# Kernel optimization log

Measured on AMD Instinct MI355X. Metric: run time of the kernel, lower is better.

The kernel has to match this reference:

```python
import jax, jax.numpy as jnp
import numpy as np

P = 16          # patch size
ER = 2          # expand_ratio = per-head dim in Hgru2

def _shift2d(x, sh, sw):
    # zero-fill shift of (B,C,H,W) image by (sh, sw); matches torch F.pad((l,r,t,b)) with a negative crop
    H, W = x.shape[2], x.shape[3]
    ah, aw = abs(sh), abs(sw)
    xp = jnp.pad(x, ((0, 0), (0, 0), (ah, ah), (aw, aw)))
    return xp[:, :, ah - sh:ah - sh + H, aw - sw:aw - sw + W]

def _layernorm(x, g, b, eps=1e-5):
    m = jnp.mean(x, axis=-1, keepdims=True)
    v = jnp.var(x, axis=-1, keepdims=True)
    return (x - m) * jax.lax.rsqrt(v + eps) * g + b

def _rmsnorm(x, eps=1e-6):
    # FastSimpleRMSNorm: weightless RMS normalization
    return x * jax.lax.rsqrt(jnp.mean(x * x, axis=-1, keepdims=True) + eps)

def _hgru2(x, lb_vec, wi, wo):
    # x: (N, T, D). NOTE: the torch module unpacks x.shape as (n, b, d), so the
    # gated linear recurrence scans over axis 0 exactly as the original does.
    N, T, D = x.shape
    H = D // ER
    feat = x @ wi                                    # (N, T, 3D)
    V, Q, Fg = jnp.split(feat, 3, axis=-1)
    V = jax.nn.gelu(V, approximate=False).reshape(N, T, H, ER)
    Q = jax.nn.gelu(Q, approximate=False).reshape(N, T, H, ER)
    Fg = jax.nn.sigmoid(Fg).reshape(N, T, H, ER)
    lb = lb_vec.reshape(H, ER)
    lam = lb + (1.0 - lb) * Fg                       # decay lambda_t in (lb, 1)
    K = 1.0 - lam
    def step(S, inp):
        q, k, v, l = inp                             # each (T, H, ER)
        # S[t,h,i,j] = lam[i] * S + k[i] * v[j]  (GLA recurrence, 2x2 state/head)
        S = l[..., None] * S + k[..., None] * v[..., None, :]
        o = jnp.einsum('thi,thij->thj', q, S)
        return S, o
    S0 = jnp.zeros((T, H, ER, ER), dtype=x.dtype)
    _, o = jax.lax.scan(step, S0, (Q, K, V, lam))    # o: (N, T, H, ER)
    return o.reshape(N, T, D) @ wo

def reference(img, spt_ln_g, spt_ln_b, spt_w, spt_b, pos_emb, cls_token, lower_bounds,
              in_proj_w, out_proj_w, ff_w1, ff_b1, ff_w2, ff_b2,
              head_ln_g, head_ln_b, head_w, head_b):
    B, C, Hh, Ww = img.shape
    # SPT: concat original + 4 shifted copies on channel axis -> (B, 5C, H, W)
    xs = jnp.concatenate([img,
                          _shift2d(img, 0, 1), _shift2d(img, 0, -1),
                          _shift2d(img, 1, 0), _shift2d(img, -1, 0)], axis=1)
    c5 = 5 * C
    h, w = Hh // P, Ww // P
    # 'b c (h p1) (w p2) -> b (h w) (p1 p2 c)'
    patches = xs.reshape(B, c5, h, P, w, P).transpose(0, 2, 4, 3, 5, 1).reshape(B, h * w, P * P * c5)
    tokens = _layernorm(patches, spt_ln_g, spt_ln_b) @ spt_w + spt_b   # (B, NP, D)
    n = tokens.shape[1]
    cls = jnp.broadcast_to(cls_token, (B, 1, tokens.shape[2]))
    x = jnp.concatenate([cls, tokens], axis=1) + pos_emb[:, :n + 1]
    # layer-wise monotone lower bounds for the decay gate
    lb = jax.nn.softmax(lower_bounds, axis=0)
    lb = jnp.cumsum(lb, axis=0)
    lb = lb - lb[0]
    depth = lower_bounds.shape[0]
    for i in range(depth):
        x = _hgru2(_rmsnorm(x), lb[i], in_proj_w[i], out_proj_w[i]) + x
        hmid = jax.nn.gelu(_rmsnorm(x) @ ff_w1[i] + ff_b1[i], approximate=False)
        x = hmid @ ff_w2[i] + ff_b2[i] + x
    x = _rmsnorm(x)
    x = x[:, 0]                                      # cls pooling
    return _layernorm(x, head_ln_g, head_ln_b) @ head_w + head_b

def setup_inputs():
    key = jax.random.key(0)
    ks = jax.random.split(key, 10)
    B, C, IMG, D, DEPTH, MLP, NC = 16, 3, 256, 768, 8, 3072, 1000
    NP = (IMG // P) ** 2
    PD = P * P * 5 * C
    s = 0.02
    return {
        'img': jax.random.normal(ks[0], (B, C, IMG, IMG), jnp.float32),
        'spt_ln_g': jnp.ones((PD,), jnp.float32),
        'spt_ln_b': jnp.zeros((PD,), jnp.float32),
        'spt_w': jax.random.normal(ks[1], (PD, D), jnp.float32) * s,
        'spt_b': jnp.zeros((D,), jnp.float32),
        'pos_emb': jax.random.normal(ks[2], (1, NP + 1, D), jnp.float32),
        'cls_token': jax.random.normal(ks[3], (1, 1, D), jnp.float32),
        'lower_bounds': jnp.ones((DEPTH, D), jnp.float32),
        'in_proj_w': jax.random.normal(ks[4], (DEPTH, D, 3 * D), jnp.float32) * s,
        'out_proj_w': jax.random.normal(ks[5], (DEPTH, D, D), jnp.float32) * s,
        'ff_w1': jax.random.normal(ks[6], (DEPTH, D, MLP), jnp.float32) * s,
        'ff_b1': jnp.zeros((DEPTH, MLP), jnp.float32),
        'ff_w2': jax.random.normal(ks[7], (DEPTH, MLP, D), jnp.float32) * s,
        'ff_b2': jnp.zeros((DEPTH, D), jnp.float32),
        'head_ln_g': jnp.ones((D,), jnp.float32),
        'head_ln_b': jnp.zeros((D,), jnp.float32),
        'head_w': jax.random.normal(ks[8], (D, NC), jnp.float32) * s,
        'head_b': jnp.zeros((NC,), jnp.float32),
    }
```

## Files before the change

### kernel.cpp

```cpp
#include <hip/hip_runtime.h>
#include <hip/hip_bf16.h>

typedef __bf16 bf16x8 __attribute__((ext_vector_type(8)));
typedef float floatx4 __attribute__((ext_vector_type(4)));

#define DEV __device__ __forceinline__

DEV float gelu_f(float x) {
    return 0.5f * x * (1.0f + erff(x * 0.70710678118654752f));
}

DEV void block_reduce2(float& a, float& b, float* s) {
    #pragma unroll
    for (int o = 32; o > 0; o >>= 1) {
        a += __shfl_down(a, o, 64);
        b += __shfl_down(b, o, 64);
    }
    __syncthreads();
    int wv = threadIdx.x >> 6;
    if ((threadIdx.x & 63) == 0) { s[wv * 2] = a; s[wv * 2 + 1] = b; }
    __syncthreads();
    int nw = blockDim.x >> 6;
    float ra = 0.f, rb = 0.f;
    for (int i = 0; i < nw; ++i) { ra += s[i * 2]; rb += s[i * 2 + 1]; }
    a = ra; b = rb;
}

__global__ __launch_bounds__(256) void compute_lb(const float* __restrict__ lbin, float* __restrict__ lbout) {
    int d = blockIdx.x * 256 + threadIdx.x;
    if (d >= 768) return;
    float v[8];
    float mx = -1e30f;
    #pragma unroll
    for (int i = 0; i < 8; ++i) { v[i] = lbin[i * 768 + d]; mx = fmaxf(mx, v[i]); }
    float s = 0.f;
    #pragma unroll
    for (int i = 0; i < 8; ++i) { v[i] = expf(v[i] - mx); s += v[i]; }
    float inv = 1.f / s;
    float first = v[0] * inv;
    float cum = 0.f;
    #pragma unroll
    for (int i = 0; i < 8; ++i) { cum += v[i] * inv; lbout[i * 768 + d] = cum - first; }
}

__global__ __launch_bounds__(256) void init_tokens(const float* __restrict__ cls, const float* __restrict__ pos,
                                                   const float* __restrict__ bias, float* __restrict__ x) {
    int i = blockIdx.x * 256 + threadIdx.x;
    if (i >= 16 * 257 * 768) return;
    int d = i % 768;
    int row = i / 768;
    int t = row % 257;
    float v;
    if (t == 0) v = cls[d] + pos[d];
    else        v = bias[d] + pos[(size_t)t * 768 + d];
    x[(size_t)row * 768 + d] = v;
}

__global__ __launch_bounds__(256) void patch_ln(const float* __restrict__ img, const float* __restrict__ g,
                                                const float* __restrict__ bt, __hip_bfloat16* __restrict__ out) {
    int pm = blockIdx.x;
    int b = pm >> 8, pp = pm & 255;
    int ph = pp >> 4, pw = pp & 15;
    __shared__ float pv[3840];
    __shared__ float sbuf[8];
    float s = 0.f, ss = 0.f;
    #pragma unroll
    for (int i = 0; i < 15; ++i) {
        int f = threadIdx.x + i * 256;
        int pi = f / 15, cc = f % 15;
        int ip = pi >> 4, jp = pi & 15;
        int g5 = cc / 3, ch = cc % 3;
        int sh = (g5 == 3) - (g5 == 4);
        int sw = (g5 == 1) - (g5 == 2);
        int y = ph * 16 + ip - sh;
        int x = pw * 16 + jp - sw;
        float val = 0.f;
        if ((unsigned)y < 256u && (unsigned)x < 256u)
            val = img[(((size_t)b * 3 + ch) * 256 + y) * 256 + x];
        pv[f] = val; s += val; ss += val * val;
    }
    block_reduce2(s, ss, sbuf);
    float mean = s * (1.f / 3840.f);
    float var  = ss * (1.f / 3840.f) - mean * mean;
    float inv  = rsqrtf(var + 1e-5f);
    #pragma unroll
    for (int i = 0; i < 15; ++i) {
        int f = threadIdx.x + i * 256;
        out[(size_t)pm * 3840 + f] = __float2bfloat16((pv[f] - mean) * inv * g[f] + bt[f]);
    }
}

__global__ __launch_bounds__(256) void transpose_cast(const float* __restrict__ W, __hip_bfloat16* __restrict__ Wt,
                                                      int K, int N) {
    __shared__ float tile[32][33];
    int k0 = blockIdx.x * 32, n0 = blockIdx.y * 32;
    int tx = threadIdx.x & 31, ty = threadIdx.x >> 5;
    #pragma unroll
    for (int i = 0; i < 4; ++i) {
        int k = ty + i * 8;
        tile[k][tx] = W[(size_t)(k0 + k) * N + n0 + tx];
    }
    __syncthreads();
    #pragma unroll
    for (int i = 0; i < 4; ++i) {
        int n = ty + i * 8;
        Wt[(size_t)(n0 + n) * K + k0 + tx] = __float2bfloat16(tile[tx][n]);
    }
}

__global__ __launch_bounds__(256) void rmsnorm_kernel(const float* __restrict__ x, __hip_bfloat16* __restrict__ out) {
    int row = blockIdx.x;
    const float* xr = x + (size_t)row * 768;
    __shared__ float sbuf[8];
    float v[3];
    float ss = 0.f, d0 = 0.f;
    #pragma unroll
    for (int i = 0; i < 3; ++i) { v[i] = xr[threadIdx.x + i * 256]; ss += v[i] * v[i]; }
    block_reduce2(ss, d0, sbuf);
    float scale = rsqrtf(ss * (1.f / 768.f) + 1e-6f);
    #pragma unroll
    for (int i = 0; i < 3; ++i)
        out[(size_t)row * 768 + threadIdx.x + i * 256] = __float2bfloat16(v[i] * scale);
}

__global__ __launch_bounds__(256) void hgru_scan(const float* __restrict__ feat, __hip_bfloat16* __restrict__ o) {
    int idx = blockIdx.x * 256 + threadIdx.x;
    if (idx >= 257 * 384) return;
    int t = idx / 384, h = idx % 384;
    float S00 = 0.f, S01 = 0.f, S10 = 0.f, S11 = 0.f;
    for (int n = 0; n < 16; ++n) {
        size_t base = ((size_t)n * 257 + t) * 2304;
        float v0 = feat[base + h * 2],        v1 = feat[base + h * 2 + 1];
        float q0 = feat[base + 768 + h * 2],  q1 = feat[base + 768 + h * 2 + 1];
        float l0 = feat[base + 1536 + h * 2], l1 = feat[base + 1536 + h * 2 + 1];
        float k0 = 1.f - l0, k1 = 1.f - l1;
        S00 = l0 * S00 + k0 * v0; S01 = l0 * S01 + k0 * v1;
        S10 = l1 * S10 + k1 * v0; S11 = l1 * S11 + k1 * v1;
        float o0 = q0 * S00 + q1 * S10;
        float o1 = q0 * S01 + q1 * S11;
        size_t ob = ((size_t)n * 257 + t) * 768 + h * 2;
        o[ob]     = __float2bfloat16(o0);
        o[ob + 1] = __float2bfloat16(o1);
    }
}

__global__ __launch_bounds__(256) void head_kernel(const float* __restrict__ x, const float* __restrict__ g,
                                                   const float* __restrict__ be, const float* __restrict__ hw,
                                                   const float* __restrict__ hb, float* __restrict__ out) {
    int b = blockIdx.x;
    const float* xr = x + (size_t)b * 257 * 768;
    __shared__ float z[768];
    __shared__ float sbuf[8];
    float v[3];
    float ss = 0.f, d0 = 0.f;
    #pragma unroll
    for (int i = 0; i < 3; ++i) { v[i] = xr[threadIdx.x + i * 256]; ss += v[i] * v[i]; }
    block_reduce2(ss, d0, sbuf);
    float rs = rsqrtf(ss * (1.f / 768.f) + 1e-6f);
    float s = 0.f, s2 = 0.f;
    #pragma unroll
    for (int i = 0; i < 3; ++i) { float y = v[i] * rs; s += y; s2 += y * y; }
    block_reduce2(s, s2, sbuf);
    float mean = s * (1.f / 768.f);
    float var  = s2 * (1.f / 768.f) - mean * mean;
    float inv  = rsqrtf(var + 1e-5f);
    #pragma unroll
    for (int i = 0; i < 3; ++i) {
        int d = threadIdx.x + i * 256;
        z[d] = (v[i] * rs - mean) * inv * g[d] + be[d];
    }
    __syncthreads();
    int j = blockIdx.y * 256 + threadIdx.x;
    if (j < 1000) {
        float acc = hb[j];
        for (int d = 0; d < 768; ++d) acc += z[d] * hw[d * 1000 + j];
        out[b * 1000 + j] = acc;
    }
}

template<int EPI, int SPLITK>
__global__ __launch_bounds__(256) void gemm_bt(
        const __hip_bfloat16* __restrict__ A, const __hip_bfloat16* __restrict__ Bt,
        int N, int Ktot, int Mvalid,
        float* __restrict__ outf, __hip_bfloat16* __restrict__ outb,
        const float* __restrict__ bias, const float* __restrict__ aux) {
    __shared__ alignas(16) __hip_bfloat16 Als[2][128 * 32];
    __shared__ alignas(16) __hip_bfloat16 Bls[2][128 * 32];
    const int tid  = threadIdx.x;
    const int lane = tid & 63;
    const int wv   = tid >> 6;
    const int m0 = blockIdx.y * 128;
    const int n0 = blockIdx.x * 128;
    const int kLen  = Ktot / SPLITK;
    const int kBase = blockIdx.z * kLen;
    const int wm = wv & 1, wn = wv >> 1;
    const int fr = lane & 15;
    const int fq = lane >> 4;
    const int srow = lane >> 2;
    const int scol = (lane & 3) * 8;

    floatx4 acc[4][4];
    #pragma unroll
    for (int mi = 0; mi < 4; ++mi)
        #pragma unroll
        for (int ni = 0; ni < 4; ++ni)
            acc[mi][ni] = (floatx4){0.f, 0.f, 0.f, 0.f};

    const int c  = wv * 2;
    const int r0 = c * 16 + srow;

    auto stage = [&](int kt, int buf) {
        #pragma unroll
        for (int j = 0; j < 2; ++j) {
            int cc = c + j;
            int r  = r0 + j * 16;
            const __hip_bfloat16* ga = A  + (size_t)(m0 + r) * Ktot + kBase + kt + scol;
            __builtin_amdgcn_global_load_lds((const __attribute__((address_space(1))) void*)ga,
                                             (__attribute__((address_space(3))) void*)(&Als[buf][cc * 512]), 16, 0, 0);
            const __hip_bfloat16* gb = Bt + (size_t)(n0 + r) * Ktot + kBase + kt + scol;
            __builtin_amdgcn_global_load_lds((const __attribute__((address_space(1))) void*)gb,
                                             (__attribute__((address_space(3))) void*)(&Bls[buf][cc * 512]), 16, 0, 0);
        }
    };

    const int nk = kLen / 32;
    stage(0, 0);
    __syncthreads();

    for (int i = 0; i < nk; ++i) {
        const int cur = i & 1;
        bf16x8 af[4], bfv[4];
        #pragma unroll
        for (int mi = 0; mi < 4; ++mi)
            af[mi] = *(const bf16x8*)((const void*)&Als[cur][(wm * 64 + mi * 16 + fr) * 32 + fq * 8]);
        #pragma unroll
        for (int ni = 0; ni < 4; ++ni)
            bfv[ni] = *(const bf16x8*)((const void*)&Bls[cur][(wn * 64 + ni * 16 + fr) * 32 + fq * 8]);
        if (i + 1 < nk) stage((i + 1) * 32, cur ^ 1);
        #pragma unroll
        for (int mi = 0; mi < 4; ++mi)
            #pragma unroll
            for (int ni = 0; ni < 4; ++ni)
                acc[mi][ni] = __builtin_amdgcn_mfma_f32_16x16x32_bf16(af[mi], bfv[ni], acc[mi][ni], 0, 0, 0);
        __syncthreads();
    }

    const int cr0 = wm * 64 + fq * 4;
    const int cc0 = wn * 64 + fr;
    #pragma unroll
    for (int mi = 0; mi < 4; ++mi) {
        #pragma unroll
        for (int r = 0; r < 4; ++r) {
            int gm = m0 + cr0 + mi * 16 + r;
            if (gm >= Mvalid) continue;
            #pragma unroll
            for (int ni = 0; ni < 4; ++ni) {
                int gn = n0 + cc0 + ni * 16;
                float v = acc[mi][ni][r];
                if (EPI == 0) {
                    int b = gm >> 8, p = gm & 255;
                    size_t orow = (size_t)b * 257 + 1 + p;
                    atomicAdd(&outf[orow * 768 + gn], v);
                } else if (EPI == 1) {
                    float res;
                    if (gn < 1536) {
                        res = gelu_f(v);
                    } else {
                        float l = aux[gn - 1536];
                        res = l + (1.f - l) / (1.f + expf(-v));
                    }
                    outf[(size_t)gm * N + gn] = res;
                } else if (EPI == 2) {
                    if (SPLITK > 1) atomicAdd(&outf[(size_t)gm * N + gn], v);
                    else            outf[(size_t)gm * N + gn] += v;
                } else if (EPI == 3) {
                    outb[(size_t)gm * N + gn] = __float2bfloat16(gelu_f(v + bias[gn]));
                } else if (EPI == 4) {
                    float add = v + (blockIdx.z == 0 ? bias[gn] : 0.f);
                    if (SPLITK > 1) atomicAdd(&outf[(size_t)gm * N + gn], add);
                    else            outf[(size_t)gm * N + gn] += add;
                }
            }
        }
    }
}

extern "C" void kernel_launch(void* const* d_in, const int* in_sizes, int n_in,
                              void* d_out, int out_size, void* d_ws, size_t ws_size,
                              hipStream_t stream) {
    const float* img        = (const float*)d_in[0];
    const float* spt_ln_g   = (const float*)d_in[1];
    const float* spt_ln_b   = (const float*)d_in[2];
    const float* spt_w      = (const float*)d_in[3];
    const float* spt_b      = (const float*)d_in[4];
    const float* pos_emb    = (const float*)d_in[5];
    const float* cls_token  = (const float*)d_in[6];
    const float* lower_bnds = (const float*)d_in[7];
    const float* in_proj_w  = (const float*)d_in[8];
    const float* out_proj_w = (const float*)d_in[9];
    const float* ff_w1      = (const float*)d_in[10];
    const float* ff_b1      = (const float*)d_in[11];
    const float* ff_w2      = (const float*)d_in[12];
    const float* ff_b2      = (const float*)d_in[13];
    const float* head_ln_g  = (const float*)d_in[14];
    const float* head_ln_b  = (const float*)d_in[15];
    const float* head_w     = (const float*)d_in[16];
    const float* head_b     = (const float*)d_in[17];
    float* out = (float*)d_out;

    char* wp = (char*)d_ws;
    auto alloc = [&](size_t bytes) -> void* {
        void* p = (void*)wp;
        wp += (bytes + 255) & ~(size_t)255;
        return p;
    };
    float*          lbbuf   = (float*)         alloc(8 * 768 * 4);
    __hip_bfloat16* patches = (__hip_bfloat16*)alloc((size_t)4096 * 3840 * 2);
    __hip_bfloat16* spt_wt  = (__hip_bfloat16*)alloc((size_t)768 * 3840 * 2);
    float*          xbuf    = (float*)         alloc((size_t)4112 * 768 * 4);
    __hip_bfloat16* normbuf = (__hip_bfloat16*)alloc((size_t)4224 * 768 * 2);
    float*          featbuf = (float*)         alloc((size_t)4112 * 2304 * 4);
    __hip_bfloat16* obuf    = (__hip_bfloat16*)alloc((size_t)4224 * 768 * 2);
    __hip_bfloat16* midbuf  = (__hip_bfloat16*)alloc((size_t)4224 * 3072 * 2);
    __hip_bfloat16* w_in_t  = (__hip_bfloat16*)alloc((size_t)2304 * 768 * 2);
    __hip_bfloat16* w_out_t = (__hip_bfloat16*)alloc((size_t)768 * 768 * 2);
    __hip_bfloat16* w1_t    = (__hip_bfloat16*)alloc((size_t)3072 * 768 * 2);
    __hip_bfloat16* w2_t    = (__hip_bfloat16*)alloc((size_t)768 * 3072 * 2);
    (void)in_sizes; (void)n_in; (void)out_size; (void)ws_size;

    compute_lb<<<3, 256, 0, stream>>>(lower_bnds, lbbuf);
    init_tokens<<<(16 * 257 * 768 + 255) / 256, 256, 0, stream>>>(cls_token, pos_emb, spt_b, xbuf);
    patch_ln<<<4096, 256, 0, stream>>>(img, spt_ln_g, spt_ln_b, patches);
    transpose_cast<<<dim3(3840 / 32, 768 / 32), 256, 0, stream>>>(spt_w, spt_wt, 3840, 768);
    gemm_bt<0, 4><<<dim3(6, 32, 4), 256, 0, stream>>>(patches, spt_wt, 768, 3840, 4096,
                                                      xbuf, nullptr, nullptr, nullptr);

    for (int i = 0; i < 8; ++i) {
        rmsnorm_kernel<<<4112, 256, 0, stream>>>(xbuf, normbuf);
        transpose_cast<<<dim3(24, 72), 256, 0, stream>>>(in_proj_w + (size_t)i * 768 * 2304, w_in_t, 768, 2304);
        gemm_bt<1, 1><<<dim3(18, 33, 1), 256, 0, stream>>>(normbuf, w_in_t, 2304, 768, 4112,
                                                           featbuf, nullptr, nullptr, lbbuf + i * 768);
        hgru_scan<<<386, 256, 0, stream>>>(featbuf, obuf);
        transpose_cast<<<dim3(24, 24), 256, 0, stream>>>(out_proj_w + (size_t)i * 768 * 768, w_out_t, 768, 768);
        gemm_bt<2, 2><<<dim3(6, 33, 2), 256, 0, stream>>>(obuf, w_out_t, 768, 768, 4112,
                                                          xbuf, nullptr, nullptr, nullptr);
        rmsnorm_kernel<<<4112, 256, 0, stream>>>(xbuf, normbuf);
        transpose_cast<<<dim3(24, 96), 256, 0, stream>>>(ff_w1 + (size_t)i * 768 * 3072, w1_t, 768, 3072);
        gemm_bt<3, 1><<<dim3(24, 33, 1), 256, 0, stream>>>(normbuf, w1_t, 3072, 768, 4112,
                                                           nullptr, midbuf, ff_b1 + i * 3072, nullptr);
        transpose_cast<<<dim3(96, 24), 256, 0, stream>>>(ff_w2 + (size_t)i * 3072 * 768, w2_t, 3072, 768);
        gemm_bt<4, 4><<<dim3(6, 33, 4), 256, 0, stream>>>(midbuf, w2_t, 768, 3072, 4112,
                                                          xbuf, nullptr, ff_b2 + i * 768, nullptr);
    }

    head_kernel<<<dim3(16, 4), 256, 0, stream>>>(xbuf, head_ln_g, head_ln_b, head_w, head_b, out);
}
```

Baseline: 2.200 ms.

## Register-staged swizzled GEMM pipeline, bf16 feature buffer, narrower out-proj tiles

The GEMM now loads the next-but-one k-tile into registers and writes it to XOR-swizzled LDS after the MFMAs, replacing the direct global-to-LDS loads. This is meant to overlap global latency with compute and avoid LDS bank conflicts. The tile width NT becomes a template parameter, so the out-proj GEMM runs with 64-wide N tiles on twice as many blocks. The in-proj epilogue writes bf16 features instead of fp32, and the scan reads them as bf16 pairs, halving that traffic at some cost in precision for the gates and values.

```diff
diff --git a/kernel.cpp b/kernel.cpp
--- a/kernel.cpp
+++ b/kernel.cpp
@@ -123,16 +123,20 @@
         out[(size_t)row * 768 + threadIdx.x + i * 256] = __float2bfloat16(v[i] * scale);
 }
 
-__global__ __launch_bounds__(256) void hgru_scan(const float* __restrict__ feat, __hip_bfloat16* __restrict__ o) {
+__global__ __launch_bounds__(256) void hgru_scan(const __hip_bfloat162* __restrict__ feat,
+                                                 __hip_bfloat16* __restrict__ o) {
     int idx = blockIdx.x * 256 + threadIdx.x;
     if (idx >= 257 * 384) return;
     int t = idx / 384, h = idx % 384;
     float S00 = 0.f, S01 = 0.f, S10 = 0.f, S11 = 0.f;
     for (int n = 0; n < 16; ++n) {
-        size_t base = ((size_t)n * 257 + t) * 2304;
-        float v0 = feat[base + h * 2],        v1 = feat[base + h * 2 + 1];
-        float q0 = feat[base + 768 + h * 2],  q1 = feat[base + 768 + h * 2 + 1];
-        float l0 = feat[base + 1536 + h * 2], l1 = feat[base + 1536 + h * 2 + 1];
+        size_t b2 = ((size_t)n * 257 + t) * 1152;
+        __hip_bfloat162 V = feat[b2 + h];
+        __hip_bfloat162 Q = feat[b2 + 384 + h];
+        __hip_bfloat162 L = feat[b2 + 768 + h];
+        float v0 = __bfloat162float(V.x), v1 = __bfloat162float(V.y);
+        float q0 = __bfloat162float(Q.x), q1 = __bfloat162float(Q.y);
+        float l0 = __bfloat162float(L.x), l1 = __bfloat162float(L.y);
         float k0 = 1.f - l0, k1 = 1.f - l1;
         S00 = l0 * S00 + k0 * v0; S01 = l0 * S01 + k0 * v1;
         S10 = l1 * S10 + k1 * v0; S11 = l1 * S11 + k1 * v1;
@@ -178,75 +182,99 @@
     }
 }
 
-template<int EPI, int SPLITK>
+template<int EPI, int SPLITK, int NT>
 __global__ __launch_bounds__(256) void gemm_bt(
         const __hip_bfloat16* __restrict__ A, const __hip_bfloat16* __restrict__ Bt,
         int N, int Ktot, int Mvalid,
         float* __restrict__ outf, __hip_bfloat16* __restrict__ outb,
         const float* __restrict__ bias, const float* __restrict__ aux) {
+    constexpr int NF = NT / 32;
+    constexpr int BJ = NT / 64;
     __shared__ alignas(16) __hip_bfloat16 Als[2][128 * 32];
-    __shared__ alignas(16) __hip_bfloat16 Bls[2][128 * 32];
+    __shared__ alignas(16) __hip_bfloat16 Bls[2][NT * 32];
     const int tid  = threadIdx.x;
     const int lane = tid & 63;
     const int wv   = tid >> 6;
     const int m0 = blockIdx.y * 128;
-    const int n0 = blockIdx.x * 128;
+    const int n0 = blockIdx.x * NT;
     const int kLen  = Ktot / SPLITK;
     const int kBase = blockIdx.z * kLen;
     const int wm = wv & 1, wn = wv >> 1;
     const int fr = lane & 15;
     const int fq = lane >> 4;
-    const int srow = lane >> 2;
-    const int scol = (lane & 3) * 8;
-
-    floatx4 acc[4][4];
+    const int sr = tid >> 2;
+    const int sc = tid & 3;
+
+    floatx4 acc[4][NF];
     #pragma unroll
     for (int mi = 0; mi < 4; ++mi)
         #pragma unroll
-        for (int ni = 0; ni < 4; ++ni)
+        for (int ni = 0; ni < NF; ++ni)
             acc[mi][ni] = (floatx4){0.f, 0.f, 0.f, 0.f};
 
-    const int c  = wv * 2;
-    const int r0 = c * 16 + srow;
-
-    auto stage = [&](int kt, int buf) {
+    int4 ra[2][2], rb[2][BJ];
+
+    auto gload = [&](int kt, int pipe) {
         #pragma unroll
         for (int j = 0; j < 2; ++j) {
-            int cc = c + j;
-            int r  = r0 + j * 16;
-            const __hip_bfloat16* ga = A  + (size_t)(m0 + r) * Ktot + kBase + kt + scol;
-            __builtin_amdgcn_global_load_lds((const __attribute__((address_space(1))) void*)ga,
-                                             (__attribute__((address_space(3))) void*)(&Als[buf][cc * 512]), 16, 0, 0);
-            const __hip_bfloat16* gb = Bt + (size_t)(n0 + r) * Ktot + kBase + kt + scol;
-            __builtin_amdgcn_global_load_lds((const __attribute__((address_space(1))) void*)gb,
-                                             (__attribute__((address_space(3))) void*)(&Bls[buf][cc * 512]), 16, 0, 0);
+            int r = sr + 64 * j;
+            ra[pipe][j] = *(const int4*)(A + (size_t)(m0 + r) * Ktot + kBase + kt + sc * 8);
+        }
+        #pragma unroll
+        for (int j = 0; j < BJ; ++j) {
+            int r = sr + 64 * j;
+            rb[pipe][j] = *(const int4*)(Bt + (size_t)(n0 + r) * Ktot + kBase + kt + sc * 8);
         }
     };
+    auto swz = [&](int row, int chunk) -> int {
+        return row * 64 + ((chunk ^ ((row >> 1) & 3)) * 16);
+    };
+    auto swrite = [&](int pipe, int buf) {
+        #pragma unroll
+        for (int j = 0; j < 2; ++j) {
+            int r = sr + 64 * j;
+            *(int4*)((char*)&Als[buf][0] + swz(r, sc)) = ra[pipe][j];
+        }
+        #pragma unroll
+        for (int j = 0; j < BJ; ++j) {
+            int r = sr + 64 * j;
+            *(int4*)((char*)&Bls[buf][0] + swz(r, sc)) = rb[pipe][j];
+        }
+    };
 
     const int nk = kLen / 32;
-    stage(0, 0);
+    gload(0, 0);
+    if (nk > 1) gload(32, 1);
+    swrite(0, 0);
     __syncthreads();
 
     for (int i = 0; i < nk; ++i) {
         const int cur = i & 1;
-        bf16x8 af[4], bfv[4];
-        #pragma unroll
-        for (int mi = 0; mi < 4; ++mi)
-            af[mi] = *(const bf16x8*)((const void*)&Als[cur][(wm * 64 + mi * 16 + fr) * 32 + fq * 8]);
-        #pragma unroll
-        for (int ni = 0; ni < 4; ++ni)
-            bfv[ni] = *(const bf16x8*)((const void*)&Bls[cur][(wn * 64 + ni * 16 + fr) * 32 + fq * 8]);
-        if (i + 1 < nk) stage((i + 1) * 32, cur ^ 1);
+        if (i + 2 < nk) gload((i + 2) * 32, cur);
+        bf16x8 af[4], bfv[NF];
+        #pragma unroll
+        for (int mi = 0; mi < 4; ++mi) {
+            int row = wm * 64 + mi * 16 + fr;
+            af[mi] = *(const bf16x8*)((const char*)&Als[cur][0] + swz(row, fq));
+        }
+        #pragma unroll
+        for (int ni = 0; ni < NF; ++ni) {
+            int row = wn * (NT / 2) + ni * 16 + fr;
+            bfv[ni] = *(const bf16x8*)((const char*)&Bls[cur][0] + swz(row, fq));
+        }
         #pragma unroll
         for (int mi = 0; mi < 4; ++mi)
             #pragma unroll
-            for (int ni = 0; ni < 4; ++ni)
+            for (int ni = 0; ni < NF; ++ni)
                 acc[mi][ni] = __builtin_amdgcn_mfma_f32_16x16x32_bf16(af[mi], bfv[ni], acc[mi][ni], 0, 0, 0);
-        __syncthreads();
+        if (i + 1 < nk) {
+            swrite(cur ^ 1, cur ^ 1);
+            __syncthreads();
+        }
     }
 
     const int cr0 = wm * 64 + fq * 4;
-    const int cc0 = wn * 64 + fr;
+    const int cc0 = wn * (NT / 2) + fr;
     #pragma unroll
     for (int mi = 0; mi < 4; ++mi) {
         #pragma unroll
@@ -254,7 +282,7 @@
             int gm = m0 + cr0 + mi * 16 + r;
             if (gm >= Mvalid) continue;
             #pragma unroll
-            for (int ni = 0; ni < 4; ++ni) {
+            for (int ni = 0; ni < NF; ++ni) {
                 int gn = n0 + cc0 + ni * 16;
                 float v = acc[mi][ni][r];
                 if (EPI == 0) {
@@ -269,7 +297,7 @@
                         float l = aux[gn - 1536];
                         res = l + (1.f - l) / (1.f + expf(-v));
                     }
-                    outf[(size_t)gm * N + gn] = res;
+                    outb[(size_t)gm * N + gn] = __float2bfloat16(res);
                 } else if (EPI == 2) {
                     if (SPLITK > 1) atomicAdd(&outf[(size_t)gm * N + gn], v);
                     else            outf[(size_t)gm * N + gn] += v;
@@ -319,7 +347,7 @@
     __hip_bfloat16* spt_wt  = (__hip_bfloat16*)alloc((size_t)768 * 3840 * 2);
     float*          xbuf    = (float*)         alloc((size_t)4112 * 768 * 4);
     __hip_bfloat16* normbuf = (__hip_bfloat16*)alloc((size_t)4224 * 768 * 2);
-    float*          featbuf = (float*)         alloc((size_t)4112 * 2304 * 4);
+    __hip_bfloat16* featbuf = (__hip_bfloat16*)alloc((size_t)4112 * 2304 * 2);
     __hip_bfloat16* obuf    = (__hip_bfloat16*)alloc((size_t)4224 * 768 * 2);
     __hip_bfloat16* midbuf  = (__hip_bfloat16*)alloc((size_t)4224 * 3072 * 2);
     __hip_bfloat16* w_in_t  = (__hip_bfloat16*)alloc((size_t)2304 * 768 * 2);
@@ -332,25 +360,25 @@
     init_tokens<<<(16 * 257 * 768 + 255) / 256, 256, 0, stream>>>(cls_token, pos_emb, spt_b, xbuf);
     patch_ln<<<4096, 256, 0, stream>>>(img, spt_ln_g, spt_ln_b, patches);
     transpose_cast<<<dim3(3840 / 32, 768 / 32), 256, 0, stream>>>(spt_w, spt_wt, 3840, 768);
-    gemm_bt<0, 4><<<dim3(6, 32, 4), 256, 0, stream>>>(patches, spt_wt, 768, 3840, 4096,
-                                                      xbuf, nullptr, nullptr, nullptr);
+    gemm_bt<0, 4, 128><<<dim3(6, 32, 4), 256, 0, stream>>>(patches, spt_wt, 768, 3840, 4096,
+                                                           xbuf, nullptr, nullptr, nullptr);
 
     for (int i = 0; i < 8; ++i) {
         rmsnorm_kernel<<<4112, 256, 0, stream>>>(xbuf, normbuf);
         transpose_cast<<<dim3(24, 72), 256, 0, stream>>>(in_proj_w + (size_t)i * 768 * 2304, w_in_t, 768, 2304);
-        gemm_bt<1, 1><<<dim3(18, 33, 1), 256, 0, stream>>>(normbuf, w_in_t, 2304, 768, 4112,
-                                                           featbuf, nullptr, nullptr, lbbuf + i * 768);
-        hgru_scan<<<386, 256, 0, stream>>>(featbuf, obuf);
+        gemm_bt<1, 1, 128><<<dim3(18, 33, 1), 256, 0, stream>>>(normbuf, w_in_t, 2304, 768, 4112,
+                                                                nullptr, featbuf, nullptr, lbbuf + i * 768);
+        hgru_scan<<<386, 256, 0, stream>>>((const __hip_bfloat162*)featbuf, obuf);
         transpose_cast<<<dim3(24, 24), 256, 0, stream>>>(out_proj_w + (size_t)i * 768 * 768, w_out_t, 768, 768);
-        gemm_bt<2, 2><<<dim3(6, 33, 2), 256, 0, stream>>>(obuf, w_out_t, 768, 768, 4112,
-                                                          xbuf, nullptr, nullptr, nullptr);
+        gemm_bt<2, 2, 64><<<dim3(12, 33, 2), 256, 0, stream>>>(obuf, w_out_t, 768, 768, 4112,
+                                                               xbuf, nullptr, nullptr, nullptr);
         rmsnorm_kernel<<<4112, 256, 0, stream>>>(xbuf, normbuf);
         transpose_cast<<<dim3(24, 96), 256, 0, stream>>>(ff_w1 + (size_t)i * 768 * 3072, w1_t, 768, 3072);
-        gemm_bt<3, 1><<<dim3(24, 33, 1), 256, 0, stream>>>(normbuf, w1_t, 3072, 768, 4112,
-                                                           nullptr, midbuf, ff_b1 + i * 3072, nullptr);
+        gemm_bt<3, 1, 128><<<dim3(24, 33, 1), 256, 0, stream>>>(normbuf, w1_t, 3072, 768, 4112,
+                                                                nullptr, midbuf, ff_b1 + i * 3072, nullptr);
         transpose_cast<<<dim3(96, 24), 256, 0, stream>>>(ff_w2 + (size_t)i * 3072 * 768, w2_t, 3072, 768);
-        gemm_bt<4, 4><<<dim3(6, 33, 4), 256, 0, stream>>>(midbuf, w2_t, 768, 3072, 4112,
-                                                          xbuf, nullptr, ff_b2 + i * 768, nullptr);
+        gemm_bt<4, 4, 128><<<dim3(6, 33, 4), 256, 0, stream>>>(midbuf, w2_t, 768, 3072, 4112,
+                                                               xbuf, nullptr, ff_b2 + i * 768, nullptr);
     }
 
     head_kernel<<<dim3(16, 4), 256, 0, stream>>>(xbuf, head_ln_g, head_ln_b, head_w, head_b, out);
```

New measurement: 4.271 ms. 94.2% more time.
